# Kernel optimization log

Measured on AMD Instinct MI355X. Metric: run time of the kernel, lower is better.

## Reference

```python
import jax, jax.numpy as jnp
import numpy as np

TEMPERATURE = 0.07
EPS = 1e-8


def _cosine_sim(a, b):
    # F.cosine_similarity(a[:,None], b[None,:], dim=-1) as a normalized matmul
    an = a / jnp.maximum(jnp.linalg.norm(a, axis=-1, keepdims=True), EPS)
    bn = b / jnp.maximum(jnp.linalg.norm(b, axis=-1, keepdims=True), EPS)
    return an @ bn.T  # [N, M]


def setup_inputs() -> dict:
    key = jax.random.key(0)
    k1, k2, k3, k4 = jax.random.split(key, 4)
    B, M, D, C = 512, 65536, 256, 10
    return {
        "q": jax.random.normal(k1, (B, D), dtype=jnp.float32),
        "labels": jax.random.randint(k2, (B,), 0, C, dtype=jnp.int64),
        "pro_memory": jax.random.normal(k3, (M, D), dtype=jnp.float32),
        "pro_labels": jax.random.randint(k4, (M,), 0, C, dtype=jnp.int64),
    }


def reference(q, labels, pro_memory, pro_labels):
    B = q.shape[0]
    # --- memory branch (adapt_to='prototype'), memory detached ---
    memory_logits = _cosine_sim(q, jax.lax.stop_gradient(pro_memory)) / TEMPERATURE  # [B, M]
    memory_targets = (labels[:, None] == pro_labels[None, :]).astype(jnp.float32)

    # --- source (in-batch) branch; second q is detached in matrix_sim ---
    src_contrast = _cosine_sim(q, jax.lax.stop_gradient(q)) / TEMPERATURE  # [B, B]
    src_max = jax.lax.stop_gradient(jnp.max(src_contrast, axis=1, keepdims=True))
    src_logits = src_contrast - src_max
    src_mask = 1.0 - jnp.eye(B, dtype=jnp.float32)  # zero the diagonal (self)
    src_targets = (labels[:, None] == labels[None, :]).astype(jnp.float32) * src_mask

    targets = jnp.concatenate([src_targets, memory_targets], axis=1)     # [B, B+M]
    logits = jnp.concatenate([src_logits, memory_logits], axis=1)        # [B, B+M]
    exp_logits = jnp.concatenate(
        [jnp.exp(src_logits) * src_mask, jnp.exp(memory_logits)], axis=1
    )
    log_prob = logits - jnp.log(exp_logits.sum(axis=1, keepdims=True))
    mean_log_prob_pos = (targets * log_prob).sum(axis=1) / targets.sum(axis=1)
    return -jnp.mean(mean_log_prob_pos)
```

## Files before the change

kernel.cpp:

```cpp
#include <hip/hip_runtime.h>
#include <stdint.h>
#include <math.h>

#define B_N 512
#define M_N 65536
#define D_N 256
#define C_N 10
#define TEMP_INV 14.285714285714286f
#define LOG2E_F 1.4426950408889634f
#define K2C (LOG2E_F * TEMP_INV)

typedef __attribute__((ext_vector_type(8))) __bf16 bf16x8;
typedef __attribute__((ext_vector_type(4))) float f32x4;

__device__ __forceinline__ unsigned short f2bf(float f) {
  unsigned int u = __float_as_uint(f);
  return (unsigned short)((u + 0x7FFFu + ((u >> 16) & 1u)) >> 16);
}
__device__ __forceinline__ float bf2f(unsigned short s) {
  return __uint_as_float(((unsigned int)s) << 16);
}

__global__ __launch_bounds__(256) void k_qnorm(const float* __restrict__ q,
                                               float* __restrict__ qn,
                                               unsigned short* __restrict__ qnb,
                                               unsigned short* __restrict__ qnbF,
                                               float* __restrict__ P,
                                               int* __restrict__ cnt,
                                               float* __restrict__ Zt,
                                               float* __restrict__ Ss,
                                               float* __restrict__ ns_,
                                               float* __restrict__ out) {
  const int tid = threadIdx.x, w = tid >> 6, l = tid & 63;
  const int g = l >> 4, qs = l & 15;
  if (blockIdx.x == 0) {
    for (int i = tid; i < C_N * D_N; i += 256) P[i] = 0.f;
    if (tid < C_N) cnt[tid] = 0;
    for (int i = tid; i < B_N; i += 256) { Zt[i] = 0.f; Ss[i] = 0.f; ns_[i] = 0.f; }
    if (tid == 0) out[0] = 0.f;
  }
  const int r = blockIdx.x * 16 + w * 4 + g;
  const float* src = q + (size_t)r * D_N;
  float4 v[4];
#pragma unroll
  for (int c = 0; c < 4; ++c) v[c] = *(const float4*)(src + qs * 4 + c * 64);
  float ss = 0.f;
#pragma unroll
  for (int c = 0; c < 4; ++c)
    ss += v[c].x * v[c].x + v[c].y * v[c].y + v[c].z * v[c].z + v[c].w * v[c].w;
  ss += __shfl_xor(ss, 1, 64);
  ss += __shfl_xor(ss, 2, 64);
  ss += __shfl_xor(ss, 4, 64);
  ss += __shfl_xor(ss, 8, 64);
  const float rv = 1.0f / fmaxf(sqrtf(ss), 1e-8f);
  float* dstf = qn + (size_t)r * D_N;
  unsigned short* dstb = qnb + (size_t)r * D_N;
#pragma unroll
  for (int c = 0; c < 4; ++c) {
    float4 o4;
    o4.x = v[c].x * rv; o4.y = v[c].y * rv; o4.z = v[c].z * rv; o4.w = v[c].w * rv;
    *(float4*)(dstf + qs * 4 + c * 64) = o4;
    ushort4 o;
    o.x = f2bf(o4.x); o.y = f2bf(o4.y); o.z = f2bf(o4.z); o.w = f2bf(o4.w);
    *(ushort4*)(dstb + qs * 4 + c * 64) = o;
    const int kc = (qs >> 1) + c * 8;
    *(ushort4*)(qnbF + (((size_t)kc * 512 + r) << 3) + (qs & 1) * 4) = o;
  }
}

__global__ __launch_bounds__(512, 6) void k_mega(const float* __restrict__ pm,
                                                 const unsigned short* __restrict__ qnb,
                                                 const unsigned short* __restrict__ qnbF,
                                                 const int* __restrict__ labels,
                                                 const int* __restrict__ pl,
                                                 float* __restrict__ Zt,
                                                 float* __restrict__ Ss,
                                                 float* __restrict__ ns_,
                                                 float* __restrict__ Zpart,
                                                 float* __restrict__ part2) {
  __shared__ __align__(16) unsigned char smem[37120];
  const int bid = blockIdx.x;
  const int tid = threadIdx.x, w = tid >> 6, lane = tid & 63;
  const int rsel = lane & 15, hi = lane >> 4;

  if (bid >= 16) {
    const int mt = bid - 16;
    unsigned short* Bs = (unsigned short*)smem;
    float* zall = (float*)(smem + 34816);
    int* plL = (int*)(smem + 36864);
    const float* Pm = pm + (size_t)mt * 64 * D_N;
    if (tid < 64) plL[tid] = pl[mt * 64 + tid];
    {
      const int g = lane >> 4, qs = lane & 15;
#pragma unroll
      for (int pass = 0; pass < 2; ++pass) {
        const int r = w * 8 + pass * 4 + g;
        const float* src = Pm + (size_t)r * D_N;
        float4 v[4];
#pragma unroll
        for (int c = 0; c < 4; ++c) v[c] = *(const float4*)(src + qs * 4 + c * 64);
        float ss = 0.f;
#pragma unroll
        for (int c = 0; c < 4; ++c)
          ss += v[c].x * v[c].x + v[c].y * v[c].y + v[c].z * v[c].z + v[c].w * v[c].w;
        ss += __shfl_xor(ss, 1, 64);
        ss += __shfl_xor(ss, 2, 64);
        ss += __shfl_xor(ss, 4, 64);
        ss += __shfl_xor(ss, 8, 64);
        const float rv = 1.0f / fmaxf(sqrtf(ss), 1e-8f);
#pragma unroll
        for (int c = 0; c < 4; ++c) {
          ushort4 o;
          o.x = f2bf(v[c].x * rv); o.y = f2bf(v[c].y * rv);
          o.z = f2bf(v[c].z * rv); o.w = f2bf(v[c].w * rv);
          *(ushort4*)((char*)Bs + r * 544 + qs * 8 + c * 128) = o;
        }
      }
    }
    __syncthreads();

#pragma unroll
    for (int bt = 0; bt < 2; ++bt) {
      f32x4 acc[2][4];
#pragma unroll
      for (int mi = 0; mi < 2; ++mi)
#pragma unroll
        for (int ni = 0; ni < 4; ++ni)
          acc[mi][ni] = (f32x4){0.f, 0.f, 0.f, 0.f};
#pragma unroll
      for (int it = 0; it < 8; ++it) {
        const int kc = it * 4 + hi;
        bf16x8 af[2], bfr[4];
#pragma unroll
        for (int mi = 0; mi < 2; ++mi) {
          const int r = bt * 256 + w * 32 + mi * 16 + rsel;
          af[mi] = *(const bf16x8*)(qnbF + (((size_t)kc * 512 + r) << 3));
        }
#pragma unroll
        for (int ni = 0; ni < 4; ++ni) {
          const int rB = ni * 16 + rsel;
          bfr[ni] = *(const bf16x8*)((const char*)Bs + rB * 544 + kc * 16);
        }
#pragma unroll
        for (int mi = 0; mi < 2; ++mi)
#pragma unroll
          for (int ni = 0; ni < 4; ++ni)
            acc[mi][ni] = __builtin_amdgcn_mfma_f32_16x16x32_bf16(af[mi], bfr[ni], acc[mi][ni], 0, 0, 0);
      }
#pragma unroll
      for (int mi = 0; mi < 2; ++mi) {
        float sv[4] = {0.f, 0.f, 0.f, 0.f};
#pragma unroll
        for (int ni = 0; ni < 4; ++ni)
#pragma unroll
          for (int rg = 0; rg < 4; ++rg)
            sv[rg] += __builtin_amdgcn_exp2f(acc[mi][ni][rg] * K2C);
#pragma unroll
        for (int rg = 0; rg < 4; ++rg) {
          float v = sv[rg];
          v += __shfl_xor(v, 1, 64);
          v += __shfl_xor(v, 2, 64);
          v += __shfl_xor(v, 4, 64);
          v += __shfl_xor(v, 8, 64);
          if (rsel == 0)
            zall[bt * 256 + w * 32 + mi * 16 + hi * 4 + rg] = v;
        }
      }
    }
    __syncthreads();
    Zpart[(size_t)mt * 512 + tid] = zall[tid];
    {
      const int dim = tid & 255, half = tid >> 8;
      float s0 = 0.f, s1 = 0.f, s2 = 0.f, s3 = 0.f, s4 = 0.f;
      float s5 = 0.f, s6 = 0.f, s7 = 0.f, s8 = 0.f, s9 = 0.f;
#pragma unroll 8
      for (int j = 0; j < 32; ++j) {
        const int r = half * 32 + j;
        const float v = bf2f(*(const unsigned short*)((const char*)Bs + r * 544 + dim * 2));
        switch (plL[r]) {
          case 0: s0 += v; break;
          case 1: s1 += v; break;
          case 2: s2 += v; break;
          case 3: s3 += v; break;
          case 4: s4 += v; break;
          case 5: s5 += v; break;
          case 6: s6 += v; break;
          case 7: s7 += v; break;
          case 8: s8 += v; break;
          default: s9 += v; break;
        }
      }
      float* dst = part2 + ((size_t)mt * 2 + half) * (C_N * D_N) + dim;
      dst[0] = s0; dst[256] = s1; dst[512] = s2; dst[768] = s3; dst[1024] = s4;
      dst[1280] = s5; dst[1536] = s6; dst[1792] = s7; dst[2048] = s8; dst[2304] = s9;
    }
  } else {
    unsigned short* As = (unsigned short*)smem;
    unsigned short* Bs2 = (unsigned short*)(smem + 16384);
    int* labR = (int*)(smem + 32768);
    int* labJ = (int*)(smem + 33280);
    float* zr = (float*)(smem + 33792);
    float* sr = (float*)(smem + 34304);
    float* nr = (float*)(smem + 34816);
    const int bt2 = bid >> 2, jt = bid & 3;
    const unsigned short* Ab = qnb + (size_t)(bt2 * 128) * D_N;
    const unsigned short* Bb = qnb + (size_t)(jt * 128) * D_N;
    if (tid < 128) {
      labR[tid] = labels[bt2 * 128 + tid];
      labJ[tid] = labels[jt * 128 + tid];
      zr[tid] = 0.f; sr[tid] = 0.f; nr[tid] = 0.f;
    }
    f32x4 acc[4][2];
#pragma unroll
    for (int mi = 0; mi < 4; ++mi)
#pragma unroll
      for (int ni = 0; ni < 2; ++ni)
        acc[mi][ni] = (f32x4){0.f, 0.f, 0.f, 0.f};
    const int wr = w >> 2, wc = w & 3;
    for (int ks = 0; ks < 4; ++ks) {
      const int kk = ks * 64;
#pragma unroll
      for (int i = 0; i < 2; ++i) {
        const int cbase = i * 512 + w * 64;
        const int c = cbase + lane;
        const int r = c >> 3;
        const int ss2 = (c & 7) ^ (r & 7);
        __builtin_amdgcn_global_load_lds(
            (const __attribute__((address_space(1))) void*)(Ab + (size_t)r * D_N + kk + ss2 * 8),
            (__attribute__((address_space(3))) void*)(As + cbase * 8), 16, 0, 0);
        __builtin_amdgcn_global_load_lds(
            (const __attribute__((address_space(1))) void*)(Bb + (size_t)r * D_N + kk + ss2 * 8),
            (__attribute__((address_space(3))) void*)(Bs2 + cbase * 8), 16, 0, 0);
      }
      __syncthreads();
#pragma unroll
      for (int ksl = 0; ksl < 2; ++ksl) {
        const int sb = ksl * 4 + hi;
        bf16x8 af[4], bfr[2];
#pragma unroll
        for (int mi = 0; mi < 4; ++mi) {
          const int r = wr * 64 + mi * 16 + rsel;
          af[mi] = *(const bf16x8*)((const char*)As + r * 128 + ((sb ^ (r & 7)) * 16));
        }
#pragma unroll
        for (int ni = 0; ni < 2; ++ni) {
          const int r = wc * 32 + ni * 16 + rsel;
          bfr[ni] = *(const bf16x8*)((const char*)Bs2 + r * 128 + ((sb ^ (r & 7)) * 16));
        }
#pragma unroll
        for (int mi = 0; mi < 4; ++mi)
#pragma unroll
          for (int ni = 0; ni < 2; ++ni)
            acc[mi][ni] = __builtin_amdgcn_mfma_f32_16x16x32_bf16(af[mi], bfr[ni], acc[mi][ni], 0, 0, 0);
      }
      __syncthreads();
    }
#pragma unroll
    for (int mi = 0; mi < 4; ++mi) {
      float zs[4] = {0.f, 0.f, 0.f, 0.f};
      float sv[4] = {0.f, 0.f, 0.f, 0.f};
      float nv[4] = {0.f, 0.f, 0.f, 0.f};
#pragma unroll
      for (int ni = 0; ni < 2; ++ni) {
        const int j_loc = wc * 32 + ni * 16 + rsel;
        const int jg = jt * 128 + j_loc;
        const int lj = labJ[j_loc];
#pragma unroll
        for (int rg_ = 0; rg_ < 4; ++rg_) {
          const int r_loc = wr * 64 + mi * 16 + hi * 4 + rg_;
          const int rg = bt2 * 128 + r_loc;
          const float lg = acc[mi][ni][rg_] * TEMP_INV - TEMP_INV;
          if (rg != jg) {
            zs[rg_] += __builtin_amdgcn_exp2f(lg * LOG2E_F);
            if (labR[r_loc] == lj) { sv[rg_] += lg; nv[rg_] += 1.f; }
          }
        }
      }
#pragma unroll
      for (int rg_ = 0; rg_ < 4; ++rg_) {
        float z = zs[rg_], s = sv[rg_], n = nv[rg_];
        z += __shfl_xor(z, 1, 64); z += __shfl_xor(z, 2, 64);
        z += __shfl_xor(z, 4, 64); z += __shfl_xor(z, 8, 64);
        s += __shfl_xor(s, 1, 64); s += __shfl_xor(s, 2, 64);
        s += __shfl_xor(s, 4, 64); s += __shfl_xor(s, 8, 64);
        n += __shfl_xor(n, 1, 64); n += __shfl_xor(n, 2, 64);
        n += __shfl_xor(n, 4, 64); n += __shfl_xor(n, 8, 64);
        if (rsel == 0) {
          const int r_loc = wr * 64 + mi * 16 + hi * 4 + rg_;
          atomicAdd(&zr[r_loc], z);
          atomicAdd(&sr[r_loc], s);
          atomicAdd(&nr[r_loc], n);
        }
      }
    }
    __syncthreads();
    if (tid < 128) {
      atomicAdd(&Zt[bt2 * 128 + tid], zr[tid]);
      atomicAdd(&Ss[bt2 * 128 + tid], sr[tid]);
      atomicAdd(&ns_[bt2 * 128 + tid], nr[tid]);
    }
  }
}

__global__ __launch_bounds__(256) void k_reduce2(const float* __restrict__ part2,
                                                 const int* __restrict__ pl,
                                                 const float* __restrict__ Zpart,
                                                 float* __restrict__ P,
                                                 int* __restrict__ cnt,
                                                 float* __restrict__ Zt) {
  const int tid = threadIdx.x, w = tid >> 6, lane = tid & 63;
  if (blockIdx.x < 40) {
    __shared__ int xs[4];
    const int c = blockIdx.x >> 2, q = blockIdx.x & 3;
    float s = 0.f;
#pragma unroll 8
    for (int i = 0; i < 512; ++i)
      s += part2[(size_t)(q * 512 + i) * (C_N * D_N) + c * 256 + tid];
    atomicAdd(&P[c * 256 + tid], s);
    int x = 0;
    const int* plq = pl + q * 16384;
#pragma unroll 8
    for (int jj = 0; jj < 64; ++jj)
      x += (plq[jj * 256 + tid] == c) ? 1 : 0;
    x += __shfl_xor(x, 32, 64);
    x += __shfl_xor(x, 16, 64);
    x += __shfl_xor(x, 8, 64);
    x += __shfl_xor(x, 4, 64);
    x += __shfl_xor(x, 2, 64);
    x += __shfl_xor(x, 1, 64);
    if (lane == 0) xs[w] = x;
    __syncthreads();
    if (tid == 0) atomicAdd(&cnt[c], xs[0] + xs[1] + xs[2] + xs[3]);
  } else {
    __shared__ float zl[4][64];
    const int zb = blockIdx.x - 40;
    const int b = zb * 64 + (tid & 63);
    const int s = tid >> 6;
    float acc = 0.f;
#pragma unroll 8
    for (int k = 0; k < 256; ++k)
      acc += Zpart[(size_t)(s * 256 + k) * 512 + b];
    zl[s][tid & 63] = acc;
    __syncthreads();
    if (tid < 64)
      Zt[zb * 64 + tid] += zl[0][tid] + zl[1][tid] + zl[2][tid] + zl[3][tid];
  }
}

__global__ __launch_bounds__(256) void k_final(const float* __restrict__ qn,
                                               const int* __restrict__ labels,
                                               const float* __restrict__ P,
                                               const int* __restrict__ cnt,
                                               const float* __restrict__ Zt,
                                               const float* __restrict__ Ss,
                                               const float* __restrict__ ns_,
                                               float* __restrict__ out) {
  __shared__ float partl[4];
  const int tid = threadIdx.x, w = tid >> 6, lane = tid & 63;
  const int b = blockIdx.x * 4 + w;
  const int cls = labels[b];
  const float4 v = *(const float4*)(qn + (size_t)b * D_N + lane * 4);
  const float4 p = *(const float4*)(P + (size_t)cls * D_N + lane * 4);
  float d = v.x * p.x + v.y * p.y + v.z * p.z + v.w * p.w;
  d += __shfl_xor(d, 32, 64);
  d += __shfl_xor(d, 16, 64);
  d += __shfl_xor(d, 8, 64);
  d += __shfl_xor(d, 4, 64);
  d += __shfl_xor(d, 2, 64);
  d += __shfl_xor(d, 1, 64);
  if (lane == 0) {
    const float smem_ = d * TEMP_INV;
    const float ntot = ns_[b] + (float)cnt[cls];
    partl[w] = (Ss[b] + smem_) / ntot - logf(Zt[b]);
  }
  __syncthreads();
  if (tid == 0)
    atomicAdd(out, -(partl[0] + partl[1] + partl[2] + partl[3]) * (1.0f / (float)B_N));
}

extern "C" void kernel_launch(void* const* d_in, const int* in_sizes, int n_in,
                              void* d_out, int out_size, void* d_ws, size_t ws_size,
                              hipStream_t stream) {
  const float* q = (const float*)d_in[0];
  const int* labels = (const int*)d_in[1];
  const float* pm = (const float*)d_in[2];
  const int* pl = (const int*)d_in[3];
  float* out = (float*)d_out;

  char* wsb = (char*)d_ws;
  float* qn = (float*)wsb;
  unsigned short* qnb = (unsigned short*)(wsb + 524288);
  unsigned short* qnbF = (unsigned short*)(wsb + 786432);
  float* P = (float*)(wsb + 1048576);
  int* cnt = (int*)(wsb + 1058816);
  float* Zt = (float*)(wsb + 1058880);
  float* Ss = (float*)(wsb + 1060928);
  float* ns_ = (float*)(wsb + 1062976);
  float* part2 = (float*)(wsb + 1065024);
  float* Zpart = (float*)(wsb + 22036544);

  k_qnorm<<<32, 256, 0, stream>>>(q, qn, qnb, qnbF, P, cnt, Zt, Ss, ns_, out);
  k_mega<<<1040, 512, 0, stream>>>(pm, qnb, qnbF, labels, pl, Zt, Ss, ns_, Zpart, part2);
  k_reduce2<<<48, 256, 0, stream>>>(part2, pl, Zpart, P, cnt, Zt);
  k_final<<<128, 256, 0, stream>>>(qn, labels, P, cnt, Zt, Ss, ns_, out);
}
```

Before: 92.59 us.

## Double memory tile per block and reuse query fragments across two halves

Each memory block now handles 128 prototype rows instead of 64, which halves the block count and the partial-sum buffers that later reductions must read. Query A-fragments are loaded once into registers per pass and reused across both 64-row halves of the memory tile, cutting repeated global reads of the normalized queries. The per-class accumulation switches from a switch statement to branchless predicated adds. In exchange, shared memory per block roughly doubles and register pressure rises, which lowers occupancy (launch bounds go from 6 to 4 waves per SIMD hint).

```diff
diff --git a/kernel.cpp b/kernel.cpp
--- a/kernel.cpp
+++ b/kernel.cpp
@@ -68,7 +68,7 @@
   }
 }
 
-__global__ __launch_bounds__(512, 6) void k_mega(const float* __restrict__ pm,
+__global__ __launch_bounds__(512, 4) void k_mega(const float* __restrict__ pm,
                                                  const unsigned short* __restrict__ qnb,
                                                  const unsigned short* __restrict__ qnbF,
                                                  const int* __restrict__ labels,
@@ -78,7 +78,7 @@
                                                  float* __restrict__ ns_,
                                                  float* __restrict__ Zpart,
                                                  float* __restrict__ part2) {
-  __shared__ __align__(16) unsigned char smem[37120];
+  __shared__ __align__(16) unsigned char smem[72192];
   const int bid = blockIdx.x;
   const int tid = threadIdx.x, w = tid >> 6, lane = tid & 63;
   const int rsel = lane & 15, hi = lane >> 4;
@@ -86,15 +86,15 @@
   if (bid >= 16) {
     const int mt = bid - 16;
     unsigned short* Bs = (unsigned short*)smem;
-    float* zall = (float*)(smem + 34816);
-    int* plL = (int*)(smem + 36864);
-    const float* Pm = pm + (size_t)mt * 64 * D_N;
-    if (tid < 64) plL[tid] = pl[mt * 64 + tid];
+    float* zall = (float*)(smem + 69632);
+    int* plL = (int*)(smem + 71680);
+    const float* Pm = pm + (size_t)mt * 128 * D_N;
+    if (tid < 128) plL[tid] = pl[mt * 128 + tid];
     {
       const int g = lane >> 4, qs = lane & 15;
 #pragma unroll
-      for (int pass = 0; pass < 2; ++pass) {
-        const int r = w * 8 + pass * 4 + g;
+      for (int pass = 0; pass < 4; ++pass) {
+        const int r = pass * 32 + w * 4 + g;
         const float* src = Pm + (size_t)r * D_N;
         float4 v[4];
 #pragma unroll
@@ -120,50 +120,54 @@
     __syncthreads();
 
 #pragma unroll
-    for (int bt = 0; bt < 2; ++bt) {
-      f32x4 acc[2][4];
-#pragma unroll
-      for (int mi = 0; mi < 2; ++mi)
-#pragma unroll
-        for (int ni = 0; ni < 4; ++ni)
-          acc[mi][ni] = (f32x4){0.f, 0.f, 0.f, 0.f};
-#pragma unroll
-      for (int it = 0; it < 8; ++it) {
-        const int kc = it * 4 + hi;
-        bf16x8 af[2], bfr[4];
+    for (int pass = 0; pass < 2; ++pass) {
+      const int qbase = pass * 256 + w * 32;
+      bf16x8 af[2][8];
+#pragma unroll
+      for (int it = 0; it < 8; ++it)
+#pragma unroll
+        for (int mi = 0; mi < 2; ++mi)
+          af[mi][it] = *(const bf16x8*)(qnbF +
+              (((size_t)(it * 4 + hi) * 512 + qbase + mi * 16 + rsel) << 3));
+#pragma unroll
+      for (int mh = 0; mh < 2; ++mh) {
+        f32x4 acc[2][4];
+#pragma unroll
+        for (int mi = 0; mi < 2; ++mi)
+#pragma unroll
+          for (int ni = 0; ni < 4; ++ni)
+            acc[mi][ni] = (f32x4){0.f, 0.f, 0.f, 0.f};
+#pragma unroll
+        for (int it = 0; it < 8; ++it) {
+          const int kc = it * 4 + hi;
+#pragma unroll
+          for (int ni = 0; ni < 4; ++ni) {
+            const int rB = mh * 64 + ni * 16 + rsel;
+            const bf16x8 bfr = *(const bf16x8*)((const char*)Bs + rB * 544 + kc * 16);
+            acc[0][ni] = __builtin_amdgcn_mfma_f32_16x16x32_bf16(af[0][it], bfr, acc[0][ni], 0, 0, 0);
+            acc[1][ni] = __builtin_amdgcn_mfma_f32_16x16x32_bf16(af[1][it], bfr, acc[1][ni], 0, 0, 0);
+          }
+        }
 #pragma unroll
         for (int mi = 0; mi < 2; ++mi) {
-          const int r = bt * 256 + w * 32 + mi * 16 + rsel;
-          af[mi] = *(const bf16x8*)(qnbF + (((size_t)kc * 512 + r) << 3));
-        }
-#pragma unroll
-        for (int ni = 0; ni < 4; ++ni) {
-          const int rB = ni * 16 + rsel;
-          bfr[ni] = *(const bf16x8*)((const char*)Bs + rB * 544 + kc * 16);
-        }
-#pragma unroll
-        for (int mi = 0; mi < 2; ++mi)
+          float sv[4] = {0.f, 0.f, 0.f, 0.f};
 #pragma unroll
           for (int ni = 0; ni < 4; ++ni)
-            acc[mi][ni] = __builtin_amdgcn_mfma_f32_16x16x32_bf16(af[mi], bfr[ni], acc[mi][ni], 0, 0, 0);
-      }
-#pragma unroll
-      for (int mi = 0; mi < 2; ++mi) {
-        float sv[4] = {0.f, 0.f, 0.f, 0.f};
-#pragma unroll
-        for (int ni = 0; ni < 4; ++ni)
-#pragma unroll
-          for (int rg = 0; rg < 4; ++rg)
-            sv[rg] += __builtin_amdgcn_exp2f(acc[mi][ni][rg] * K2C);
-#pragma unroll
-        for (int rg = 0; rg < 4; ++rg) {
-          float v = sv[rg];
-          v += __shfl_xor(v, 1, 64);
-          v += __shfl_xor(v, 2, 64);
-          v += __shfl_xor(v, 4, 64);
-          v += __shfl_xor(v, 8, 64);
-          if (rsel == 0)
-            zall[bt * 256 + w * 32 + mi * 16 + hi * 4 + rg] = v;
+#pragma unroll
+            for (int rg = 0; rg < 4; ++rg)
+              sv[rg] += __builtin_amdgcn_exp2f(acc[mi][ni][rg] * K2C);
+#pragma unroll
+          for (int rg = 0; rg < 4; ++rg) {
+            float v = sv[rg];
+            v += __shfl_xor(v, 1, 64);
+            v += __shfl_xor(v, 2, 64);
+            v += __shfl_xor(v, 4, 64);
+            v += __shfl_xor(v, 8, 64);
+            if (rsel == 0) {
+              const int qi = qbase + mi * 16 + hi * 4 + rg;
+              if (mh == 0) zall[qi] = v; else zall[qi] += v;
+            }
+          }
         }
       }
     }
@@ -173,22 +177,21 @@
       const int dim = tid & 255, half = tid >> 8;
       float s0 = 0.f, s1 = 0.f, s2 = 0.f, s3 = 0.f, s4 = 0.f;
       float s5 = 0.f, s6 = 0.f, s7 = 0.f, s8 = 0.f, s9 = 0.f;
-#pragma unroll 8
-      for (int j = 0; j < 32; ++j) {
-        const int r = half * 32 + j;
+#pragma unroll 4
+      for (int j = 0; j < 64; ++j) {
+        const int r = half * 64 + j;
         const float v = bf2f(*(const unsigned short*)((const char*)Bs + r * 544 + dim * 2));
-        switch (plL[r]) {
-          case 0: s0 += v; break;
-          case 1: s1 += v; break;
-          case 2: s2 += v; break;
-          case 3: s3 += v; break;
-          case 4: s4 += v; break;
-          case 5: s5 += v; break;
-          case 6: s6 += v; break;
-          case 7: s7 += v; break;
-          case 8: s8 += v; break;
-          default: s9 += v; break;
-        }
+        const int cls = plL[r];
+        s0 += (cls == 0) ? v : 0.f;
+        s1 += (cls == 1) ? v : 0.f;
+        s2 += (cls == 2) ? v : 0.f;
+        s3 += (cls == 3) ? v : 0.f;
+        s4 += (cls == 4) ? v : 0.f;
+        s5 += (cls == 5) ? v : 0.f;
+        s6 += (cls == 6) ? v : 0.f;
+        s7 += (cls == 7) ? v : 0.f;
+        s8 += (cls == 8) ? v : 0.f;
+        s9 += (cls == 9) ? v : 0.f;
       }
       float* dst = part2 + ((size_t)mt * 2 + half) * (C_N * D_N) + dim;
       dst[0] = s0; dst[256] = s1; dst[512] = s2; dst[768] = s3; dst[1024] = s4;
@@ -314,8 +317,8 @@
     const int c = blockIdx.x >> 2, q = blockIdx.x & 3;
     float s = 0.f;
 #pragma unroll 8
-    for (int i = 0; i < 512; ++i)
-      s += part2[(size_t)(q * 512 + i) * (C_N * D_N) + c * 256 + tid];
+    for (int i = 0; i < 256; ++i)
+      s += part2[(size_t)(q * 256 + i) * (C_N * D_N) + c * 256 + tid];
     atomicAdd(&P[c * 256 + tid], s);
     int x = 0;
     const int* plq = pl + q * 16384;
@@ -338,8 +341,8 @@
     const int s = tid >> 6;
     float acc = 0.f;
 #pragma unroll 8
-    for (int k = 0; k < 256; ++k)
-      acc += Zpart[(size_t)(s * 256 + k) * 512 + b];
+    for (int k = 0; k < 128; ++k)
+      acc += Zpart[(size_t)(s * 128 + k) * 512 + b];
     zl[s][tid & 63] = acc;
     __syncthreads();
     if (tid < 64)
@@ -397,10 +400,10 @@
   float* Ss = (float*)(wsb + 1060928);
   float* ns_ = (float*)(wsb + 1062976);
   float* part2 = (float*)(wsb + 1065024);
-  float* Zpart = (float*)(wsb + 22036544);
+  float* Zpart = (float*)(wsb + 11550784);
 
   k_qnorm<<<32, 256, 0, stream>>>(q, qn, qnb, qnbF, P, cnt, Zt, Ss, ns_, out);
-  k_mega<<<1040, 512, 0, stream>>>(pm, qnb, qnbF, labels, pl, Zt, Ss, ns_, Zpart, part2);
+  k_mega<<<528, 512, 0, stream>>>(pm, qnb, qnbF, labels, pl, Zt, Ss, ns_, Zpart, part2);
   k_reduce2<<<48, 256, 0, stream>>>(part2, pl, Zpart, P, cnt, Zt);
   k_final<<<128, 256, 0, stream>>>(qn, labels, P, cnt, Zt, Ss, ns_, out);
 }
```

After: 75.61 us (median of 4 runs). 18.3% less time.

## Retile memory-branch MFMA to a 64-row warp tile over all queries

Applied to the files above, without the earlier changes.

The memory-branch GEMM changes from two passes of 32 rows per warp into a single pass in which each warp owns 64 query rows and all 64 prototype columns. Each B fragment loaded from LDS is now reused across four MFMAs, and A fragments are loaded in batches of eight per k-chunk. This roughly halves LDS B reads, but the larger accumulator tile pushes register use up, so the launch-bounds occupancy hint drops from 6 to 2. The class-sum loop also swaps its switch for predicated selects, and several loops are pinned to no unrolling.

```diff
diff --git a/kernel.cpp b/kernel.cpp
--- a/kernel.cpp
+++ b/kernel.cpp
@@ -68,7 +68,7 @@
   }
 }
 
-__global__ __launch_bounds__(512, 6) void k_mega(const float* __restrict__ pm,
+__global__ __launch_bounds__(512, 2) void k_mega(const float* __restrict__ pm,
                                                  const unsigned short* __restrict__ qnb,
                                                  const unsigned short* __restrict__ qnbF,
                                                  const int* __restrict__ labels,
@@ -92,9 +92,9 @@
     if (tid < 64) plL[tid] = pl[mt * 64 + tid];
     {
       const int g = lane >> 4, qs = lane & 15;
-#pragma unroll
+#pragma unroll 1
       for (int pass = 0; pass < 2; ++pass) {
-        const int r = w * 8 + pass * 4 + g;
+        const int r = pass * 32 + w * 4 + g;
         const float* src = Pm + (size_t)r * D_N;
         float4 v[4];
 #pragma unroll
@@ -119,52 +119,52 @@
     }
     __syncthreads();
 
-#pragma unroll
-    for (int bt = 0; bt < 2; ++bt) {
-      f32x4 acc[2][4];
-#pragma unroll
-      for (int mi = 0; mi < 2; ++mi)
-#pragma unroll
-        for (int ni = 0; ni < 4; ++ni)
-          acc[mi][ni] = (f32x4){0.f, 0.f, 0.f, 0.f};
-#pragma unroll
-      for (int it = 0; it < 8; ++it) {
-        const int kc = it * 4 + hi;
-        bf16x8 af[2], bfr[4];
-#pragma unroll
-        for (int mi = 0; mi < 2; ++mi) {
-          const int r = bt * 256 + w * 32 + mi * 16 + rsel;
-          af[mi] = *(const bf16x8*)(qnbF + (((size_t)kc * 512 + r) << 3));
-        }
+    f32x4 acc[4][4];
+#pragma unroll
+    for (int mi = 0; mi < 4; ++mi)
+#pragma unroll
+      for (int ni = 0; ni < 4; ++ni)
+        acc[mi][ni] = (f32x4){0.f, 0.f, 0.f, 0.f};
+#pragma unroll 1
+    for (int kh = 0; kh < 4; ++kh) {
+      bf16x8 af[8];
+#pragma unroll
+      for (int itl = 0; itl < 2; ++itl)
+#pragma unroll
+        for (int mi = 0; mi < 4; ++mi)
+          af[itl * 4 + mi] = *(const bf16x8*)(qnbF +
+              (((size_t)(kh * 8 + itl * 4 + hi) * 512 + w * 64 + mi * 16 + rsel) << 3));
+      __builtin_amdgcn_sched_barrier(0);
+#pragma unroll
+      for (int itl = 0; itl < 2; ++itl) {
+        const int kc = kh * 8 + itl * 4 + hi;
 #pragma unroll
         for (int ni = 0; ni < 4; ++ni) {
-          const int rB = ni * 16 + rsel;
-          bfr[ni] = *(const bf16x8*)((const char*)Bs + rB * 544 + kc * 16);
-        }
-#pragma unroll
-        for (int mi = 0; mi < 2; ++mi)
-#pragma unroll
-          for (int ni = 0; ni < 4; ++ni)
-            acc[mi][ni] = __builtin_amdgcn_mfma_f32_16x16x32_bf16(af[mi], bfr[ni], acc[mi][ni], 0, 0, 0);
-      }
-#pragma unroll
-      for (int mi = 0; mi < 2; ++mi) {
-        float sv[4] = {0.f, 0.f, 0.f, 0.f};
-#pragma unroll
-        for (int ni = 0; ni < 4; ++ni)
-#pragma unroll
-          for (int rg = 0; rg < 4; ++rg)
-            sv[rg] += __builtin_amdgcn_exp2f(acc[mi][ni][rg] * K2C);
-#pragma unroll
-        for (int rg = 0; rg < 4; ++rg) {
-          float v = sv[rg];
-          v += __shfl_xor(v, 1, 64);
-          v += __shfl_xor(v, 2, 64);
-          v += __shfl_xor(v, 4, 64);
-          v += __shfl_xor(v, 8, 64);
-          if (rsel == 0)
-            zall[bt * 256 + w * 32 + mi * 16 + hi * 4 + rg] = v;
-        }
+          const bf16x8 b = *(const bf16x8*)((const char*)Bs + (ni * 16 + rsel) * 544 + kc * 16);
+          acc[0][ni] = __builtin_amdgcn_mfma_f32_16x16x32_bf16(af[itl * 4 + 0], b, acc[0][ni], 0, 0, 0);
+          acc[1][ni] = __builtin_amdgcn_mfma_f32_16x16x32_bf16(af[itl * 4 + 1], b, acc[1][ni], 0, 0, 0);
+          acc[2][ni] = __builtin_amdgcn_mfma_f32_16x16x32_bf16(af[itl * 4 + 2], b, acc[2][ni], 0, 0, 0);
+          acc[3][ni] = __builtin_amdgcn_mfma_f32_16x16x32_bf16(af[itl * 4 + 3], b, acc[3][ni], 0, 0, 0);
+        }
+      }
+    }
+#pragma unroll
+    for (int mi = 0; mi < 4; ++mi) {
+      float sv[4] = {0.f, 0.f, 0.f, 0.f};
+#pragma unroll
+      for (int ni = 0; ni < 4; ++ni)
+#pragma unroll
+        for (int rg = 0; rg < 4; ++rg)
+          sv[rg] += __builtin_amdgcn_exp2f(acc[mi][ni][rg] * K2C);
+#pragma unroll
+      for (int rg = 0; rg < 4; ++rg) {
+        float v = sv[rg];
+        v += __shfl_xor(v, 1, 64);
+        v += __shfl_xor(v, 2, 64);
+        v += __shfl_xor(v, 4, 64);
+        v += __shfl_xor(v, 8, 64);
+        if (rsel == 0)
+          zall[w * 64 + mi * 16 + hi * 4 + rg] = v;
       }
     }
     __syncthreads();
@@ -173,21 +173,28 @@
       const int dim = tid & 255, half = tid >> 8;
       float s0 = 0.f, s1 = 0.f, s2 = 0.f, s3 = 0.f, s4 = 0.f;
       float s5 = 0.f, s6 = 0.f, s7 = 0.f, s8 = 0.f, s9 = 0.f;
-#pragma unroll 8
-      for (int j = 0; j < 32; ++j) {
-        const int r = half * 32 + j;
-        const float v = bf2f(*(const unsigned short*)((const char*)Bs + r * 544 + dim * 2));
-        switch (plL[r]) {
-          case 0: s0 += v; break;
-          case 1: s1 += v; break;
-          case 2: s2 += v; break;
-          case 3: s3 += v; break;
-          case 4: s4 += v; break;
-          case 5: s5 += v; break;
-          case 6: s6 += v; break;
-          case 7: s7 += v; break;
-          case 8: s8 += v; break;
-          default: s9 += v; break;
+#pragma unroll 1
+      for (int j0 = 0; j0 < 32; j0 += 4) {
+        float v[4];
+        int cl[4];
+#pragma unroll
+        for (int u = 0; u < 4; ++u) {
+          const int r = half * 32 + j0 + u;
+          v[u] = bf2f(*(const unsigned short*)((const char*)Bs + r * 544 + dim * 2));
+          cl[u] = plL[r];
+        }
+#pragma unroll
+        for (int u = 0; u < 4; ++u) {
+          s0 += (cl[u] == 0) ? v[u] : 0.f;
+          s1 += (cl[u] == 1) ? v[u] : 0.f;
+          s2 += (cl[u] == 2) ? v[u] : 0.f;
+          s3 += (cl[u] == 3) ? v[u] : 0.f;
+          s4 += (cl[u] == 4) ? v[u] : 0.f;
+          s5 += (cl[u] == 5) ? v[u] : 0.f;
+          s6 += (cl[u] == 6) ? v[u] : 0.f;
+          s7 += (cl[u] == 7) ? v[u] : 0.f;
+          s8 += (cl[u] == 8) ? v[u] : 0.f;
+          s9 += (cl[u] == 9) ? v[u] : 0.f;
         }
       }
       float* dst = part2 + ((size_t)mt * 2 + half) * (C_N * D_N) + dim;
@@ -217,6 +224,7 @@
       for (int ni = 0; ni < 2; ++ni)
         acc[mi][ni] = (f32x4){0.f, 0.f, 0.f, 0.f};
     const int wr = w >> 2, wc = w & 3;
+#pragma unroll 1
     for (int ks = 0; ks < 4; ++ks) {
       const int kk = ks * 64;
 #pragma unroll
@@ -233,7 +241,7 @@
             (__attribute__((address_space(3))) void*)(Bs2 + cbase * 8), 16, 0, 0);
       }
       __syncthreads();
-#pragma unroll
+#pragma unroll 1
       for (int ksl = 0; ksl < 2; ++ksl) {
         const int sb = ksl * 4 + hi;
         bf16x8 af[4], bfr[2];
```

Result: slower. 97.88 us (+5.7%).
